# Performance work log

Hardware: AMD Instinct MI355X
Metric: run time of the kernel (lower is better)

The kernel has to match this reference:

```python
import jax, jax.numpy as jnp
import numpy as np
import math

B, N, K, H = 2, 2048, 1024, 16
S = K // H  # head dim = 64


def apply_rope(t):
    # t: [b, h, N, s] -> rotary position embedding (rotate-half convention)
    s = t.shape[-1]
    pos = jnp.arange(t.shape[2], dtype=jnp.float32)
    inv_freq = 1.0 / (10000.0 ** (jnp.arange(0, s, 2, dtype=jnp.float32) / s))
    ang = pos[:, None] * inv_freq[None, :]               # [N, s/2]
    cos = jnp.concatenate([jnp.cos(ang), jnp.cos(ang)], axis=-1)  # [N, s]
    sin = jnp.concatenate([jnp.sin(ang), jnp.sin(ang)], axis=-1)
    t1, t2 = t[..., : s // 2], t[..., s // 2:]
    rot = jnp.concatenate([-t2, t1], axis=-1)
    return t * cos + rot * sin


def setup_inputs() -> dict:
    key = jax.random.key(0)
    ks = jax.random.split(key, 6)
    sc = 1.0 / math.sqrt(K)
    x = jax.random.normal(ks[0], (B, N, K), dtype=jnp.float32)
    Wq = jax.random.normal(ks[1], (K, K), dtype=jnp.float32) * sc
    Wk = jax.random.normal(ks[2], (K, K), dtype=jnp.float32) * sc
    Wv = jax.random.normal(ks[3], (K, K), dtype=jnp.float32) * sc
    Wu = jax.random.normal(ks[4], (K, K), dtype=jnp.float32) * sc
    bu = jax.random.normal(ks[5], (K,), dtype=jnp.float32) * 0.01
    mask = jnp.tril(jnp.ones((N, N), dtype=jnp.int32))  # causal
    return {"x": x, "Wq": Wq, "Wk": Wk, "Wv": Wv, "Wu": Wu, "bu": bu, "mask": mask}


def reference(x, Wq, Wk, Wv, Wu, bu, mask):
    b, n, k = x.shape
    h, s = H, S
    # torch Linear: y = x @ W.T
    def proj(W):
        return (x @ W.T).reshape(b, n, h, s).transpose(0, 2, 1, 3)  # [b,h,n,s]
    Q = apply_rope(proj(Wq))
    Kh = apply_rope(proj(Wk))
    V = proj(Wv)
    scores = jnp.einsum('bhqs,bhks->bhqk', Q, Kh) / math.sqrt(s)
    scores = jnp.where(mask[None, None, :, :] == 0, -jnp.inf, scores)
    attn = jax.nn.softmax(scores, axis=-1)
    out = jnp.einsum('bhqk,bhks->bhqs', attn, V)           # [b,h,n,s]
    out = out.transpose(0, 2, 1, 3).reshape(b, n, k)
    return out @ Wu.T + bu
```

## Files before the change

kernel.cpp:

```cpp
#include <hip/hip_runtime.h>
#include <hip/hip_bf16.h>

#define Bq 2
#define Nq 2048
#define Kq 1024
#define Hq 16
#define Sq 64
#define Mq (Bq * Nq)

typedef __attribute__((ext_vector_type(4))) float f32x4;
typedef __attribute__((ext_vector_type(8))) short bf16x8;

__device__ unsigned short g_xb[(size_t)Mq * Kq];
__device__ unsigned short g_Wqb[Kq * Kq];
__device__ unsigned short g_Wkb[Kq * Kq];
__device__ unsigned short g_Wvb[Kq * Kq];
__device__ unsigned short g_Wub[Kq * Kq];
__device__ unsigned short g_Qb[(size_t)Bq * Hq * Nq * Sq];
__device__ unsigned short g_Kb[(size_t)Bq * Hq * Nq * Sq];
__device__ unsigned short g_Vt[(size_t)Bq * Hq * Sq * Nq];
__device__ unsigned short g_Ao[(size_t)Mq * Kq];
__device__ __align__(16) float g_On[(size_t)32 * 16 * 3 * 128 * 64];
__device__ float g_Ol[32 * 16 * 3 * 128];

__constant__ signed char c_qt[30] = {15,15,15,14,14,14,13,13,13,12,12,12,11,11,10,10,9,9,8,8,7,7,6,6,5,4,3,2,1,0};
__constant__ signed char c_t0[30] = {0,11,22,0,10,20,0,10,19,0,9,18,0,12,0,11,0,10,0,9,0,8,0,7,0,0,0,0,0,0};
__constant__ signed char c_t1[30] = {11,22,32,10,20,30,10,19,28,9,18,26,12,24,11,22,10,20,9,18,8,16,7,14,12,10,8,6,4,2};
__constant__ signed char c_sp[30] = {0,1,2,0,1,2,0,1,2,0,1,2,0,1,0,1,0,1,0,1,0,1,0,1,0,0,0,0,0,0};
__constant__ signed char c_ns[30] = {3,3,3,3,3,3,3,3,3,3,3,3,2,2,2,2,2,2,2,2,2,2,2,2,1,1,1,1,1,1};

__device__ __forceinline__ unsigned short f2bf(float f) {
    union { float f; unsigned int i; } u; u.f = f;
    unsigned int r = u.i + 0x7FFF + ((u.i >> 16) & 1);
    return (unsigned short)(r >> 16);
}
__device__ __forceinline__ float bf2f(unsigned short u) {
    union { unsigned int i; float f; } v; v.i = ((unsigned int)u) << 16;
    return v.f;
}
__device__ __forceinline__ void async16(const unsigned short* g, unsigned short* l) {
    __builtin_amdgcn_global_load_lds(
        (const __attribute__((address_space(1))) void*)g,
        (__attribute__((address_space(3))) void*)l, 16, 0, 0);
}

__global__ __launch_bounds__(256) void convert_all_kernel(
    const float* __restrict__ x,  const float* __restrict__ wq,
    const float* __restrict__ wk, const float* __restrict__ wv,
    const float* __restrict__ wu)
{
    int i = blockIdx.x * 256 + threadIdx.x;
    const float* src; unsigned short* dst; int off;
    if (i < 1048576) { src = x; dst = g_xb; off = i; }
    else {
        int j = i - 1048576;
        int which = j >> 18;
        off = j & 262143;
        src = (which == 0) ? wq : (which == 1) ? wk : (which == 2) ? wv : wu;
        dst = (which == 0) ? g_Wqb : (which == 1) ? g_Wkb : (which == 2) ? g_Wvb : g_Wub;
    }
    float4 v = ((const float4*)src)[off];
    ushort4 o;
    o.x = f2bf(v.x); o.y = f2bf(v.y); o.z = f2bf(v.z); o.w = f2bf(v.w);
    ((ushort4*)dst)[off] = o;
}

__global__ __launch_bounds__(256) void qkv_gemm_kernel()
{
    __shared__ __align__(16) unsigned short SLDS[24576];
    auto As = (unsigned short (*)[128][32])(SLDS);
    auto Bs = (unsigned short (*)[128][32])(SLDS + 12288);

    const int n0 = blockIdx.x * 128;
    const int m0 = blockIdx.y * 128;
    const int which = n0 >> 10;
    const unsigned short* A  = g_xb;
    const unsigned short* Bm = (which == 0) ? g_Wqb : (which == 1) ? g_Wkb : g_Wvb;
    unsigned short* dst      = (which == 0) ? g_Qb : g_Kb;
    const int nb = n0 & 1023;

    const int tid = threadIdx.x;
    const int w = tid >> 6, l = tid & 63;
    const int lane16 = l & 15, quad = l >> 4;
    const int wm = (w >> 1) * 64, wn = (w & 1) * 64;

    const int sr  = l >> 2;
    const int sc  = ((l & 3) ^ ((l >> 3) & 3)) * 8;
    const int rsw = (lane16 >> 1) & 3;

    f32x4 acc[4][4];
#pragma unroll
    for (int mi = 0; mi < 4; ++mi)
#pragma unroll
        for (int ni = 0; ni < 4; ++ni) acc[mi][ni] = (f32x4){0.f, 0.f, 0.f, 0.f};

#define QSTAGE(t, b)                                                            \
    do {                                                                        \
        _Pragma("unroll")                                                       \
        for (int c = 0; c < 2; ++c) {                                           \
            async16(A  + (size_t)(m0 + 32 * w + 16 * c + sr) * Kq + (t) * 32 + sc, \
                    &As[(b)][32 * w + 16 * c][0]);                              \
            async16(Bm + (size_t)(nb + 32 * w + 16 * c + sr) * Kq + (t) * 32 + sc, \
                    &Bs[(b)][32 * w + 16 * c][0]);                              \
        }                                                                       \
    } while (0)

    QSTAGE(0, 0);
    QSTAGE(1, 1);
    asm volatile("s_waitcnt vmcnt(4)" ::: "memory");
    __builtin_amdgcn_s_barrier();
    __builtin_amdgcn_sched_barrier(0);

    int cur = 0;
    for (int kb = 0; kb < 32; ++kb) {
        if (kb + 2 < 32) QSTAGE(kb + 2, (kb + 2) % 3);

        bf16x8 af[4], bfr[4];
#pragma unroll
        for (int mi = 0; mi < 4; ++mi)
            af[mi]  = *(const bf16x8*)&As[cur][wm + mi * 16 + lane16][(quad ^ rsw) * 8];
#pragma unroll
        for (int ni = 0; ni < 4; ++ni)
            bfr[ni] = *(const bf16x8*)&Bs[cur][wn + ni * 16 + lane16][(quad ^ rsw) * 8];
#pragma unroll
        for (int mi = 0; mi < 4; ++mi)
#pragma unroll
            for (int ni = 0; ni < 4; ++ni)
                acc[mi][ni] = __builtin_amdgcn_mfma_f32_16x16x32_bf16(af[mi], bfr[ni], acc[mi][ni], 0, 0, 0);

        __builtin_amdgcn_sched_barrier(0);
        if (kb + 2 < 32) {
            asm volatile("s_waitcnt vmcnt(4)" ::: "memory");
        } else {
            asm volatile("s_waitcnt vmcnt(0)" ::: "memory");
        }
        __builtin_amdgcn_s_barrier();
        __builtin_amdgcn_sched_barrier(0);
        cur = (cur == 2) ? 0 : cur + 1;
    }
#undef QSTAGE

    const int h0 = (n0 & 1023) >> 6;
    if (which < 2) {
        const float invf0 = exp2f((float)lane16 * -0.41524101f);
        const float invf1 = exp2f((float)(lane16 + 16) * -0.41524101f);
        const int h = h0 + (wn >> 6);
#pragma unroll
        for (int mi = 0; mi < 4; ++mi)
#pragma unroll
            for (int r = 0; r < 4; ++r) {
                int m = m0 + wm + mi * 16 + quad * 4 + r;
                int b = m >> 11, nn = m & 2047;
                float np = (float)nn;
                float a0 = np * invf0, a1 = np * invf1;
                float s0 = __sinf(a0), c0 = __cosf(a0);
                float s1 = __sinf(a1), c1 = __cosf(a1);
                float t10 = acc[mi][0][r], t20 = acc[mi][2][r];
                float t11 = acc[mi][1][r], t21 = acc[mi][3][r];
                unsigned short* dr = dst + (((size_t)b * Hq + h) * Nq + nn) * Sq + lane16;
                dr[0]  = f2bf(t10 * c0 - t20 * s0);
                dr[16] = f2bf(t11 * c1 - t21 * s1);
                dr[32] = f2bf(t20 * c0 + t10 * s0);
                dr[48] = f2bf(t21 * c1 + t11 * s1);
            }
    } else {
        unsigned short* T = SLDS;
#pragma unroll
        for (int mi = 0; mi < 4; ++mi)
#pragma unroll
            for (int ni = 0; ni < 4; ++ni)
#pragma unroll
                for (int r = 0; r < 4; ++r) {
                    int nl = wn + ni * 16 + lane16;
                    int ml = wm + mi * 16 + quad * 4 + r;
                    T[nl * 136 + ml] = f2bf(acc[mi][ni][r]);
                }
        __syncthreads();
        const int b = m0 >> 11, mcol = m0 & 2047;
#pragma unroll
        for (int rr = 0; rr < 4; ++rr) {
            int row = rr * 32 + (tid >> 3);
            int h = h0 + (row >> 6), s = row & 63;
            unsigned short* drow = g_Vt + (((size_t)b * Hq + h) * Sq + s) * Nq + mcol;
#pragma unroll
            for (int ci = 0; ci < 2; ++ci) {
                int c = ci * 8 + (tid & 7);
                *(uint4*)(drow + c * 8) = *(const uint4*)(T + row * 136 + c * 8);
            }
        }
    }
}

__global__ __launch_bounds__(512) void attn_kernel()
{
    const int bh = blockIdx.x;
    const int y  = blockIdx.y;
    const int qt  = c_qt[y];
    const int t0  = c_t0[y];
    const int t1  = c_t1[y];
    const int sp  = c_sp[y];
    const int nsp = c_ns[y];
    const int q0 = qt * 128;
    const unsigned short* Qp = g_Qb + (size_t)bh * Nq * Sq;
    const unsigned short* Kp = g_Kb + (size_t)bh * Nq * Sq;
    const unsigned short* Vp = g_Vt + (size_t)bh * Sq * Nq;

    __shared__ __align__(16) unsigned short Ks[3][64][64];
    __shared__ __align__(16) unsigned short Vs[3][64][64];
    __shared__ __align__(16) unsigned short Ps[128][64];
    unsigned short* psf = &Ps[0][0];

    const int tid = threadIdx.x;
    const int w = tid >> 6, l = tid & 63;
    const int lane16 = l & 15, quad = l >> 4;
    const int sr = l >> 3;
    const int sc = ((l & 7) ^ sr) * 8;
    const int rsw = (lane16 & 7);

    bf16x8 be;
    {
        short o = (lane16 == 0) ? (short)0x3F80 : (short)0;
#pragma unroll
        for (int i = 0; i < 8; ++i) be[i] = o;
    }

    const int qlo = q0 + 16 * w;
    bf16x8 aq0 = *(const bf16x8*)(Qp + (size_t)(qlo + lane16) * Sq + quad * 8);
    bf16x8 aq1 = *(const bf16x8*)(Qp + (size_t)(qlo + lane16) * Sq + quad * 8 + 32);
    asm volatile("" : "+v"(aq0), "+v"(aq1));

    f32x4 Oacc[4];
    f32x4 Oext = (f32x4){0.f, 0.f, 0.f, 0.f};
#pragma unroll
    for (int ds = 0; ds < 4; ++ds) Oacc[ds] = (f32x4){0.f, 0.f, 0.f, 0.f};

    const float C1 = 0.18033688f;
    const float C2 = 11.54156036f;

#define STAGE(t, b)                                                           \
    do {                                                                      \
        int kn_ = (t) * 64;                                                   \
        async16(Kp + (size_t)(kn_ + 8 * w + sr) * Sq + sc, &Ks[(b)][8 * w][0]);\
        async16(Vp + (size_t)(8 * w + sr) * Nq + kn_ + sc, &Vs[(b)][8 * w][0]);\
    } while (0)

    STAGE(t0, 0);
    STAGE(t0 + 1, 1);
    asm volatile("s_waitcnt vmcnt(2)" ::: "memory");
    __builtin_amdgcn_s_barrier();
    __builtin_amdgcn_sched_barrier(0);

    int cur = 0;
    for (int kb = t0; kb < t1; ++kb) {
        if (kb + 2 < t1) STAGE(kb + 2, (kb - t0 + 2) % 3);

        if (kb * 64 <= qlo + 15) {
            f32x4 S[4];
#pragma unroll
            for (int kc = 0; kc < 4; ++kc) S[kc] = (f32x4){0.f, 0.f, 0.f, 0.f};
#pragma unroll
            for (int kc = 0; kc < 4; ++kc) {
                const unsigned short* krow = &Ks[cur][kc * 16 + lane16][0];
                bf16x8 bk0 = *(const bf16x8*)&krow[(quad ^ rsw) * 8];
                bf16x8 bk1 = *(const bf16x8*)&krow[((4 + quad) ^ rsw) * 8];
                S[kc] = __builtin_amdgcn_mfma_f32_16x16x32_bf16(aq0, bk0, S[kc], 0, 0, 0);
                S[kc] = __builtin_amdgcn_mfma_f32_16x16x32_bf16(aq1, bk1, S[kc], 0, 0, 0);
            }

            const int qbase = qlo + quad * 4;
            if (kb * 64 + 63 > qlo) {
#pragma unroll
                for (int kc = 0; kc < 4; ++kc) {
                    int kpos = kb * 64 + kc * 16 + lane16;
#pragma unroll
                    for (int r = 0; r < 4; ++r)
                        S[kc][r] = (kpos <= qbase + r) ? exp2f(fmaf(S[kc][r], C1, -C2)) : 0.0f;
                }
            } else {
#pragma unroll
                for (int kc = 0; kc < 4; ++kc)
#pragma unroll
                    for (int r = 0; r < 4; ++r)
                        S[kc][r] = exp2f(fmaf(S[kc][r], C1, -C2));
            }

#pragma unroll
            for (int kc = 0; kc < 4; ++kc)
#pragma unroll
                for (int r = 0; r < 4; ++r) {
                    int prow = 16 * w + quad * 4 + r;
                    psf[(prow * 64 + kc * 16 + lane16) ^ ((prow & 7) << 3)] =
                        (unsigned short)(__float_as_uint(S[kc][r]) >> 16);
                }

            const int prow2 = 16 * w + lane16;
#pragma unroll
            for (int kk = 0; kk < 2; ++kk) {
                bf16x8 pa = *(const bf16x8*)(psf +
                    ((prow2 * 64 + kk * 32 + quad * 8) ^ (rsw << 3)));
#pragma unroll
                for (int ds = 0; ds < 4; ++ds) {
                    bf16x8 vb = *(const bf16x8*)&Vs[cur][ds * 16 + lane16][((kk * 4 + quad) ^ rsw) * 8];
                    Oacc[ds] = __builtin_amdgcn_mfma_f32_16x16x32_bf16(pa, vb, Oacc[ds], 0, 0, 0);
                }
                Oext = __builtin_amdgcn_mfma_f32_16x16x32_bf16(pa, be, Oext, 0, 0, 0);
            }
        }

        __builtin_amdgcn_sched_barrier(0);
        if (kb + 2 < t1) {
            asm volatile("s_waitcnt vmcnt(2)" ::: "memory");
        } else {
            asm volatile("s_waitcnt vmcnt(0)" ::: "memory");
        }
        __builtin_amdgcn_s_barrier();
        __builtin_amdgcn_sched_barrier(0);
        cur = (cur == 2) ? 0 : cur + 1;
    }
#undef STAGE

    if (nsp == 1) {
        const int b = bh >> 4, h = bh & 15;
        float inv[4];
#pragma unroll
        for (int r = 0; r < 4; ++r) {
            float lr = __shfl(Oext[r], quad * 16, 64);
            inv[r] = 1.0f / lr;
        }
#pragma unroll
        for (int ds = 0; ds < 4; ++ds)
#pragma unroll
            for (int r = 0; r < 4; ++r) {
                int nn = qlo + quad * 4 + r;
                g_Ao[((size_t)b * Nq + nn) * Kq + h * Sq + ds * 16 + lane16] =
                    f2bf(Oacc[ds][r] * inv[r]);
            }
    } else {
        float* On = g_On + (((size_t)bh * 16 + qt) * 3 + sp) * (128 * 64);
        float* Ol = g_Ol + (((size_t)bh * 16 + qt) * 3 + sp) * 128;
#pragma unroll
        for (int r = 0; r < 4; ++r) {
            float lr = __shfl(Oext[r], quad * 16, 64);
            if (lane16 == 0) Ol[16 * w + quad * 4 + r] = lr;
        }
#pragma unroll
        for (int ds = 0; ds < 4; ++ds)
#pragma unroll
            for (int r = 0; r < 4; ++r)
                On[(16 * w + quad * 4 + r) * 64 + ds * 16 + lane16] = Oacc[ds][r];
    }
}

__global__ __launch_bounds__(256) void attn_combine_kernel()
{
    const int bh = blockIdx.x;
    const int qt = 6 + blockIdx.y;
    const int nsp = (qt >= 12) ? 3 : 2;
    const int tid = threadIdx.x;
    const int row = tid >> 1;
    const int ch  = (tid & 1) * 32;
    const size_t sb = ((size_t)bh * 16 + qt) * 3;
    const float* On0 = g_On + (sb + 0) * (128 * 64);
    const float* On1 = g_On + (sb + 1) * (128 * 64);
    const float* On2 = g_On + (sb + 2) * (128 * 64);
    const float* Ol  = g_Ol + sb * 128;

    float lsum = Ol[row] + Ol[128 + row];
    if (nsp == 3) lsum += Ol[256 + row];
    float inv = 1.0f / lsum;

    const int b = bh >> 4, h = bh & 15, nn = qt * 128 + row;
    unsigned short* dst = g_Ao + ((size_t)b * Nq + nn) * Kq + h * Sq + ch;

#pragma unroll
    for (int j = 0; j < 8; ++j) {
        int o = row * 64 + ch + j * 4;
        f32x4 v = *(const f32x4*)(On0 + o);
        v += *(const f32x4*)(On1 + o);
        if (nsp == 3) v += *(const f32x4*)(On2 + o);
        ushort4 u;
        u.x = f2bf(v[0] * inv); u.y = f2bf(v[1] * inv);
        u.z = f2bf(v[2] * inv); u.w = f2bf(v[3] * inv);
        ((ushort4*)dst)[j] = u;
    }
}

__global__ __launch_bounds__(256) void out_gemm_kernel(
    const float* __restrict__ bu, float* __restrict__ out)
{
    __shared__ __align__(16) unsigned short As[2][128][64];
    __shared__ __align__(16) unsigned short Bs[2][128][64];

    const int n0 = blockIdx.x * 128;
    const int m0 = blockIdx.y * 128;

    const int tid = threadIdx.x;
    const int w = tid >> 6, l = tid & 63;
    const int lane16 = l & 15, quad = l >> 4;
    const int wm = (w >> 1) * 64, wn = (w & 1) * 64;
    const int sr = l >> 3;
    const int sc = ((l & 7) ^ sr) * 8;
    const int rsw = (lane16 & 7);

    f32x4 acc[4][4];
#pragma unroll
    for (int mi = 0; mi < 4; ++mi)
#pragma unroll
        for (int ni = 0; ni < 4; ++ni) acc[mi][ni] = (f32x4){0.f, 0.f, 0.f, 0.f};

#pragma unroll
    for (int c = 0; c < 4; ++c) {
        async16(g_Ao  + (size_t)(m0 + 32 * w + 8 * c + sr) * Kq + sc, &As[0][32 * w + 8 * c][0]);
        async16(g_Wub + (size_t)(n0 + 32 * w + 8 * c + sr) * Kq + sc, &Bs[0][32 * w + 8 * c][0]);
    }
    __syncthreads();

    int cur = 0;
    for (int kt = 0; kt < Kq; kt += 64) {
        if (kt + 64 < Kq) {
            int nxt = cur ^ 1;
#pragma unroll
            for (int c = 0; c < 4; ++c) {
                async16(g_Ao  + (size_t)(m0 + 32 * w + 8 * c + sr) * Kq + kt + 64 + sc, &As[nxt][32 * w + 8 * c][0]);
                async16(g_Wub + (size_t)(n0 + 32 * w + 8 * c + sr) * Kq + kt + 64 + sc, &Bs[nxt][32 * w + 8 * c][0]);
            }
        }
#pragma unroll
        for (int ks = 0; ks < 2; ++ks) {
            bf16x8 af[4], bfr[4];
#pragma unroll
            for (int mi = 0; mi < 4; ++mi)
                af[mi]  = *(const bf16x8*)&As[cur][wm + mi * 16 + lane16][((ks * 4 + quad) ^ rsw) * 8];
#pragma unroll
            for (int ni = 0; ni < 4; ++ni)
                bfr[ni] = *(const bf16x8*)&Bs[cur][wn + ni * 16 + lane16][((ks * 4 + quad) ^ rsw) * 8];
#pragma unroll
            for (int mi = 0; mi < 4; ++mi)
#pragma unroll
                for (int ni = 0; ni < 4; ++ni)
                    acc[mi][ni] = __builtin_amdgcn_mfma_f32_16x16x32_bf16(af[mi], bfr[ni], acc[mi][ni], 0, 0, 0);
        }
        __syncthreads();
        cur ^= 1;
    }

#pragma unroll
    for (int mi = 0; mi < 4; ++mi)
#pragma unroll
        for (int ni = 0; ni < 4; ++ni)
#pragma unroll
            for (int r = 0; r < 4; ++r) {
                int m = m0 + wm + mi * 16 + quad * 4 + r;
                int n = n0 + wn + ni * 16 + lane16;
                out[(size_t)m * Kq + n] = acc[mi][ni][r] + bu[n];
            }
}

extern "C" void kernel_launch(void* const* d_in, const int* in_sizes, int n_in,
                              void* d_out, int out_size, void* d_ws, size_t ws_size,
                              hipStream_t stream)
{
    const float* x  = (const float*)d_in[0];
    const float* Wq = (const float*)d_in[1];
    const float* Wk = (const float*)d_in[2];
    const float* Wv = (const float*)d_in[3];
    const float* Wu = (const float*)d_in[4];
    const float* bu = (const float*)d_in[5];
    float* out = (float*)d_out;

    convert_all_kernel<<<8192, 256, 0, stream>>>(x, Wq, Wk, Wv, Wu);
    qkv_gemm_kernel<<<dim3(24, 32), 256, 0, stream>>>();
    attn_kernel<<<dim3(32, 30), 512, 0, stream>>>();
    attn_combine_kernel<<<dim3(32, 10), 256, 0, stream>>>();
    out_gemm_kernel<<<dim3(8, 32), 256, 0, stream>>>(bu, out);
}
```

Baseline: 224.8 us.

## Enlarge QKV GEMM tiles to 256x256x64 with 512 threads and interleaved staging

The QKV projection GEMM moves from 128x128 tiles with 256 threads and a triple-buffered K=32 pipeline to 256x256 tiles with 512 threads, K=64 steps and double buffering. Global-to-LDS copies for the next step are spread across four compute sub-phases, with barriers and raised wave priority around the MFMA groups. The aim is more data reuse per tile and better overlap of loads with math. The trade-offs are 128KB of LDS and heavier register use per block. The grid shrinks to 192 blocks, fewer than the 256 CUs, so some CUs sit idle. The V transpose epilogue now runs in two passes through the LDS buffer.

Measured after the change: 215.8 us. -4.0%, faster.

```diff
diff --git a/kernel.cpp b/kernel.cpp
--- a/kernel.cpp
+++ b/kernel.cpp
@@ -65,98 +65,119 @@
     ((ushort4*)dst)[off] = o;
 }
 
-__global__ __launch_bounds__(256) void qkv_gemm_kernel()
+__global__ __launch_bounds__(512, 2) void qkv_gemm_kernel()
 {
-    __shared__ __align__(16) unsigned short SLDS[24576];
-    auto As = (unsigned short (*)[128][32])(SLDS);
-    auto Bs = (unsigned short (*)[128][32])(SLDS + 12288);
-
-    const int n0 = blockIdx.x * 128;
-    const int m0 = blockIdx.y * 128;
+    __shared__ __align__(16) unsigned short SLDS[65536];
+    auto As = (unsigned short (*)[256][64])(SLDS);
+    auto Bs = (unsigned short (*)[256][64])(SLDS + 32768);
+
+    const int n0 = blockIdx.x * 256;
+    const int m0 = blockIdx.y * 256;
     const int which = n0 >> 10;
     const unsigned short* A  = g_xb;
     const unsigned short* Bm = (which == 0) ? g_Wqb : (which == 1) ? g_Wkb : g_Wvb;
-    unsigned short* dst      = (which == 0) ? g_Qb : g_Kb;
     const int nb = n0 & 1023;
 
     const int tid = threadIdx.x;
     const int w = tid >> 6, l = tid & 63;
     const int lane16 = l & 15, quad = l >> 4;
-    const int wm = (w >> 1) * 64, wn = (w & 1) * 64;
-
-    const int sr  = l >> 2;
-    const int sc  = ((l & 3) ^ ((l >> 3) & 3)) * 8;
-    const int rsw = (lane16 >> 1) & 3;
-
-    f32x4 acc[4][4];
-#pragma unroll
-    for (int mi = 0; mi < 4; ++mi)
-#pragma unroll
-        for (int ni = 0; ni < 4; ++ni) acc[mi][ni] = (f32x4){0.f, 0.f, 0.f, 0.f};
-
-#define QSTAGE(t, b)                                                            \
-    do {                                                                        \
-        _Pragma("unroll")                                                       \
-        for (int c = 0; c < 2; ++c) {                                           \
-            async16(A  + (size_t)(m0 + 32 * w + 16 * c + sr) * Kq + (t) * 32 + sc, \
-                    &As[(b)][32 * w + 16 * c][0]);                              \
-            async16(Bm + (size_t)(nb + 32 * w + 16 * c + sr) * Kq + (t) * 32 + sc, \
-                    &Bs[(b)][32 * w + 16 * c][0]);                              \
-        }                                                                       \
-    } while (0)
-
-    QSTAGE(0, 0);
-    QSTAGE(1, 1);
-    asm volatile("s_waitcnt vmcnt(4)" ::: "memory");
+    const int wr = w >> 2, wc = w & 3;
+    const int sr8 = l >> 3;
+    const int sc  = ((l & 7) ^ sr8) * 8;
+    const int rsw = lane16 & 7;
+
+    f32x4 acc[8][4];
+#pragma unroll
+    for (int mf = 0; mf < 8; ++mf)
+#pragma unroll
+        for (int nf = 0; nf < 4; ++nf) acc[mf][nf] = (f32x4){0.f, 0.f, 0.f, 0.f};
+
+#define STG_A(t, b, c) async16(A  + (size_t)(m0 + (c)*64 + w*8 + sr8) * Kq + (t)*64 + sc, \
+                               &As[(b)][(c)*64 + w*8][0])
+#define STG_B(t, b, c) async16(Bm + (size_t)(nb + (c)*64 + w*8 + sr8) * Kq + (t)*64 + sc, \
+                               &Bs[(b)][(c)*64 + w*8][0])
+
+    STG_B(0, 0, 0); STG_B(0, 0, 1); STG_B(0, 0, 2); STG_B(0, 0, 3);
+    STG_A(0, 0, 0); STG_A(0, 0, 2); STG_A(0, 0, 1); STG_A(0, 0, 3);
+    asm volatile("s_waitcnt vmcnt(2)" ::: "memory");
     __builtin_amdgcn_s_barrier();
-    __builtin_amdgcn_sched_barrier(0);
 
     int cur = 0;
-    for (int kb = 0; kb < 32; ++kb) {
-        if (kb + 2 < 32) QSTAGE(kb + 2, (kb + 2) % 3);
-
-        bf16x8 af[4], bfr[4];
-#pragma unroll
-        for (int mi = 0; mi < 4; ++mi)
-            af[mi]  = *(const bf16x8*)&As[cur][wm + mi * 16 + lane16][(quad ^ rsw) * 8];
-#pragma unroll
-        for (int ni = 0; ni < 4; ++ni)
-            bfr[ni] = *(const bf16x8*)&Bs[cur][wn + ni * 16 + lane16][(quad ^ rsw) * 8];
-#pragma unroll
-        for (int mi = 0; mi < 4; ++mi)
-#pragma unroll
-            for (int ni = 0; ni < 4; ++ni)
-                acc[mi][ni] = __builtin_amdgcn_mfma_f32_16x16x32_bf16(af[mi], bfr[ni], acc[mi][ni], 0, 0, 0);
-
-        __builtin_amdgcn_sched_barrier(0);
-        if (kb + 2 < 32) {
-            asm volatile("s_waitcnt vmcnt(4)" ::: "memory");
-        } else {
-            asm volatile("s_waitcnt vmcnt(0)" ::: "memory");
-        }
-        __builtin_amdgcn_s_barrier();
-        __builtin_amdgcn_sched_barrier(0);
-        cur = (cur == 2) ? 0 : cur + 1;
-    }
-#undef QSTAGE
-
-    const int h0 = (n0 & 1023) >> 6;
+    for (int t = 0; t < 16; ++t) {
+        const bool stg = (t + 1 < 16);
+        const int nxt = cur ^ 1;
+        bf16x8 bf[4][2];
+#pragma unroll
+        for (int q = 0; q < 4; ++q) {
+            asm volatile("" ::: "memory");
+            bf16x8 af[2][2];
+            if (q == 0) {
+#pragma unroll
+                for (int nf = 0; nf < 4; ++nf)
+#pragma unroll
+                    for (int ks = 0; ks < 2; ++ks)
+                        bf[nf][ks] = *(const bf16x8*)
+                            &Bs[cur][wc * 64 + nf * 16 + lane16][((ks * 4 + quad) ^ rsw) * 8];
+            }
+#pragma unroll
+            for (int m2 = 0; m2 < 2; ++m2)
+#pragma unroll
+                for (int ks = 0; ks < 2; ++ks)
+                    af[m2][ks] = *(const bf16x8*)
+                        &As[cur][wr * 128 + (q * 2 + m2) * 16 + lane16][((ks * 4 + quad) ^ rsw) * 8];
+            if (stg) {
+                if (q == 0) { STG_B(t + 1, nxt, 0); STG_B(t + 1, nxt, 1); }
+                if (q == 1) { STG_B(t + 1, nxt, 2); STG_B(t + 1, nxt, 3); }
+                if (q == 2) { STG_A(t + 1, nxt, 0); STG_A(t + 1, nxt, 2); }
+                if (q == 3) { STG_A(t + 1, nxt, 1); STG_A(t + 1, nxt, 3); }
+            }
+            asm volatile("" ::: "memory");
+            __builtin_amdgcn_s_barrier();
+            asm volatile("s_waitcnt lgkmcnt(0)" ::: "memory");
+            __builtin_amdgcn_sched_barrier(0);
+            __builtin_amdgcn_s_setprio(1);
+#pragma unroll
+            for (int m2 = 0; m2 < 2; ++m2)
+#pragma unroll
+                for (int nf = 0; nf < 4; ++nf)
+#pragma unroll
+                    for (int ks = 0; ks < 2; ++ks)
+                        acc[q * 2 + m2][nf] = __builtin_amdgcn_mfma_f32_16x16x32_bf16(
+                            af[m2][ks], bf[nf][ks], acc[q * 2 + m2][nf], 0, 0, 0);
+            __builtin_amdgcn_s_setprio(0);
+            if (q == 1) {
+                if (stg) asm volatile("s_waitcnt vmcnt(4)" ::: "memory");
+                else     asm volatile("s_waitcnt vmcnt(0)" ::: "memory");
+            }
+            if (q == 3) {
+                if (stg) asm volatile("s_waitcnt vmcnt(2)" ::: "memory");
+                else     asm volatile("s_waitcnt vmcnt(0)" ::: "memory");
+            }
+            __builtin_amdgcn_s_barrier();
+        }
+        cur ^= 1;
+    }
+#undef STG_A
+#undef STG_B
+
+    const int h0q = nb >> 6;
     if (which < 2) {
+        unsigned short* dst = (which == 0) ? g_Qb : g_Kb;
+        const int h = h0q + wc;
         const float invf0 = exp2f((float)lane16 * -0.41524101f);
         const float invf1 = exp2f((float)(lane16 + 16) * -0.41524101f);
-        const int h = h0 + (wn >> 6);
-#pragma unroll
-        for (int mi = 0; mi < 4; ++mi)
+#pragma unroll
+        for (int mf = 0; mf < 8; ++mf)
 #pragma unroll
             for (int r = 0; r < 4; ++r) {
-                int m = m0 + wm + mi * 16 + quad * 4 + r;
+                int m = m0 + wr * 128 + mf * 16 + quad * 4 + r;
                 int b = m >> 11, nn = m & 2047;
                 float np = (float)nn;
                 float a0 = np * invf0, a1 = np * invf1;
                 float s0 = __sinf(a0), c0 = __cosf(a0);
                 float s1 = __sinf(a1), c1 = __cosf(a1);
-                float t10 = acc[mi][0][r], t20 = acc[mi][2][r];
-                float t11 = acc[mi][1][r], t21 = acc[mi][3][r];
+                float t10 = acc[mf][0][r], t20 = acc[mf][2][r];
+                float t11 = acc[mf][1][r], t21 = acc[mf][3][r];
                 unsigned short* dr = dst + (((size_t)b * Hq + h) * Nq + nn) * Sq + lane16;
                 dr[0]  = f2bf(t10 * c0 - t20 * s0);
                 dr[16] = f2bf(t11 * c1 - t21 * s1);
@@ -165,27 +186,30 @@
             }
     } else {
         unsigned short* T = SLDS;
-#pragma unroll
-        for (int mi = 0; mi < 4; ++mi)
-#pragma unroll
-            for (int ni = 0; ni < 4; ++ni)
-#pragma unroll
-                for (int r = 0; r < 4; ++r) {
-                    int nl = wn + ni * 16 + lane16;
-                    int ml = wm + mi * 16 + quad * 4 + r;
-                    T[nl * 136 + ml] = f2bf(acc[mi][ni][r]);
-                }
-        __syncthreads();
         const int b = m0 >> 11, mcol = m0 & 2047;
 #pragma unroll
-        for (int rr = 0; rr < 4; ++rr) {
-            int row = rr * 32 + (tid >> 3);
-            int h = h0 + (row >> 6), s = row & 63;
-            unsigned short* drow = g_Vt + (((size_t)b * Hq + h) * Sq + s) * Nq + mcol;
-#pragma unroll
-            for (int ci = 0; ci < 2; ++ci) {
-                int c = ci * 8 + (tid & 7);
-                *(uint4*)(drow + c * 8) = *(const uint4*)(T + row * 136 + c * 8);
+        for (int pass = 0; pass < 2; ++pass) {
+            __syncthreads();
+            if (wr == pass) {
+#pragma unroll
+                for (int mf = 0; mf < 8; ++mf)
+#pragma unroll
+                    for (int nf = 0; nf < 4; ++nf)
+#pragma unroll
+                        for (int r = 0; r < 4; ++r)
+                            T[(wc * 64 + nf * 16 + lane16) * 136 + mf * 16 + quad * 4 + r] =
+                                f2bf(acc[mf][nf][r]);
+            }
+            __syncthreads();
+            {
+                int row = tid >> 1;
+                int h = h0q + (row >> 6), s = row & 63;
+                unsigned short* drow = g_Vt + (((size_t)b * Hq + h) * Sq + s) * Nq
+                                        + mcol + pass * 128 + (tid & 1) * 64;
+                const unsigned short* srow = T + row * 136 + (tid & 1) * 64;
+#pragma unroll
+                for (int jj = 0; jj < 8; ++jj)
+                    *(uint4*)(drow + jj * 8) = *(const uint4*)(srow + jj * 8);
             }
         }
     }
@@ -469,7 +493,7 @@
     float* out = (float*)d_out;
 
     convert_all_kernel<<<8192, 256, 0, stream>>>(x, Wq, Wk, Wv, Wu);
-    qkv_gemm_kernel<<<dim3(24, 32), 256, 0, stream>>>();
+    qkv_gemm_kernel<<<dim3(12, 16), 512, 0, stream>>>();
     attn_kernel<<<dim3(32, 30), 512, 0, stream>>>();
     attn_combine_kernel<<<dim3(32, 10), 256, 0, stream>>>();
     out_gemm_kernel<<<dim3(8, 32), 256, 0, stream>>>(bu, out);
```
